# Optimization experiments

Measured on AMD Instinct MI355X. Metric: run time of the kernel, lower is better.

The kernel has to match this reference:

```python
import jax, jax.numpy as jnp
import numpy as np

B, S, H = 2, 2048, 2048
NH, NKV, HD = 16, 4, 128
EPS = 1e-6


def setup_inputs() -> dict:
    key = jax.random.key(0)
    ks = jax.random.split(key, 8)
    s = 0.02
    x = jax.random.normal(ks[0], (B, S, H), dtype=jnp.float32)
    # real rotary tables: cos/sin of shape [S, HD]
    inv_freq = 1.0 / (10000.0 ** (np.arange(0, HD, 2, dtype=np.float32) / HD))
    t = np.arange(S, dtype=np.float32)
    freqs = np.outer(t, inv_freq)              # [S, HD/2]
    emb = np.concatenate([freqs, freqs], axis=-1)  # [S, HD]
    rotary_cos = jnp.asarray(np.cos(emb))
    rotary_sin = jnp.asarray(np.sin(emb))
    Wq = jax.random.normal(ks[1], (H, NH * HD), dtype=jnp.float32) * s
    Wk = jax.random.normal(ks[2], (H, NKV * HD), dtype=jnp.float32) * s
    Wv = jax.random.normal(ks[3], (H, NKV * HD), dtype=jnp.float32) * s
    Wo = jax.random.normal(ks[4], (H, H), dtype=jnp.float32) * s
    q_norm_w = jnp.ones((HD,), dtype=jnp.float32)
    k_norm_w = jnp.ones((HD,), dtype=jnp.float32)
    return {"x": x, "rotary_cos": rotary_cos, "rotary_sin": rotary_sin,
            "Wq": Wq, "Wk": Wk, "Wv": Wv, "Wo": Wo,
            "q_norm_w": q_norm_w, "k_norm_w": k_norm_w}


def _rms_norm(x, w):
    return x * jax.lax.rsqrt(jnp.mean(x * x, axis=-1, keepdims=True) + EPS) * w


def _rotate_half(x):
    half = x.shape[-1] // 2
    return jnp.concatenate([-x[..., half:], x[..., :half]], axis=-1)


def reference(x, rotary_cos, rotary_sin, Wq, Wk, Wv, Wo, q_norm_w, k_norm_w):
    b, s, _ = x.shape
    q = (x @ Wq).reshape(b, s, NH, HD)
    k = (x @ Wk).reshape(b, s, NKV, HD)
    v = (x @ Wv).reshape(b, s, NKV, HD)
    q = _rms_norm(q, q_norm_w)
    k = _rms_norm(k, k_norm_w)
    cos = rotary_cos[None, :, None, :]  # [1,S,1,HD]
    sin = rotary_sin[None, :, None, :]
    q = q * cos + _rotate_half(q) * sin
    k = k * cos + _rotate_half(k) * sin
    # GQA: repeat kv heads
    rep = NH // NKV
    k = jnp.repeat(k, rep, axis=2)  # [b,s,NH,HD]
    v = jnp.repeat(v, rep, axis=2)
    scores = jnp.einsum('bqhd,bkhd->bhqk', q, k) / jnp.sqrt(jnp.float32(HD))
    causal = jnp.tril(jnp.ones((s, s), dtype=bool))
    scores = jnp.where(causal[None, None], scores, -jnp.inf)
    probs = jax.nn.softmax(scores.astype(jnp.float32), axis=-1).astype(q.dtype)
    y = jnp.einsum('bhqk,bkhd->bqhd', probs, v).reshape(b, s, NH * HD)
    return y @ Wo
```

## Files before the change

### kernel.cpp

```cpp
#include <hip/hip_runtime.h>


#define S_LEN 2048

typedef __bf16 bf16_t;
typedef bf16_t bf16x8 __attribute__((ext_vector_type(8)));
typedef float f32x4 __attribute__((ext_vector_type(4)));
typedef float f32x16 __attribute__((ext_vector_type(16)));
typedef unsigned int u32x4 __attribute__((ext_vector_type(4)));
typedef unsigned short u16x4 __attribute__((ext_vector_type(4)));

__device__ __forceinline__ unsigned short f2bf(float f) {
  unsigned int u = __builtin_bit_cast(unsigned int, f);
  u += 0x7fffu + ((u >> 16) & 1u);
  return (unsigned short)(u >> 16);
}
__device__ __forceinline__ float bf2f(unsigned short h) {
  return __builtin_bit_cast(float, (unsigned int)h << 16);
}
__device__ __forceinline__ unsigned pk2(float a, float b) {
  return (unsigned)f2bf(a) | ((unsigned)f2bf(b) << 16);
}
__device__ __forceinline__ unsigned cvtpk(float a, float b) {
  unsigned r;
  asm("v_cvt_pk_bf16_f32 %0, %1, %2" : "=v"(r) : "v"(a), "v"(b));
  return r;
}

typedef const __attribute__((address_space(1))) unsigned int* gas1_t;
typedef __attribute__((address_space(3))) unsigned int* las3_t;
__device__ __forceinline__ void async16(const void* g, void* l) {
  __builtin_amdgcn_global_load_lds((gas1_t)g, (las3_t)l, 16, 0, 0);
}

__device__ __forceinline__ bf16x8 ldfrag(const void* p) {
  return __builtin_bit_cast(bf16x8, *(const u32x4*)p);
}
__device__ __forceinline__ f32x16 mfma32(bf16x8 a, bf16x8 b, f32x16 c) {
  return __builtin_amdgcn_mfma_f32_32x32x16_bf16(a, b, c, 0, 0, 0);
}
__device__ __forceinline__ f32x16 zero16() {
  f32x16 v;
#pragma unroll
  for (int i = 0; i < 16; i++) v[i] = 0.f;
  return v;
}

__device__ __forceinline__ void transpose_body(
    const float* __restrict__ in, unsigned short* __restrict__ out,
    int C, int out_row_off, int out_ld, int bx, int by, int t,
    unsigned short (*L)[68]) {
  int r0 = by * 64, c0 = bx * 64;
#pragma unroll
  for (int i = 0; i < 4; i++) {
    int r = i * 16 + (t >> 4);
    int c = (t & 15) * 4;
    f32x4 v = *(const f32x4*)&in[(size_t)(r0 + r) * C + c0 + c];
    u16x4 u;
    u.x = f2bf(v.x); u.y = f2bf(v.y); u.z = f2bf(v.z); u.w = f2bf(v.w);
    *(u16x4*)&L[r][c] = u;
  }
  __syncthreads();
#pragma unroll
  for (int i = 0; i < 4; i++) {
    int oc = i * 16 + (t >> 4);
    int orr = (t & 15) * 4;
    u16x4 u;
    u.x = L[orr + 0][oc]; u.y = L[orr + 1][oc];
    u.z = L[orr + 2][oc]; u.w = L[orr + 3][oc];
    *(u16x4*)&out[(size_t)(c0 + oc + out_row_off) * out_ld + r0 + orr] = u;
  }
}

__global__ __launch_bounds__(256) void prep_kernel(
    const float* __restrict__ x, const float* __restrict__ Wq,
    const float* __restrict__ Wk, const float* __restrict__ Wv,
    const float* __restrict__ Wo, unsigned short* __restrict__ xb,
    unsigned short* __restrict__ WT, unsigned short* __restrict__ WoT) {
  __shared__ unsigned short L[64][68];
  const int bid = blockIdx.x, t = threadIdx.x;
  if (bid < 4096) {
    int i = bid * 256 + t;
    const f32x4* p = (const f32x4*)x + (size_t)i * 2;
    f32x4 a = p[0], b = p[1];
    u32x4 o;
    o.x = pk2(a.x, a.y);
    o.y = pk2(a.z, a.w);
    o.z = pk2(b.x, b.y);
    o.w = pk2(b.z, b.w);
    *(u32x4*)(xb + (size_t)i * 8) = o;
  } else if (bid < 5120) {
    int id = bid - 4096;
    transpose_body(Wq, WT, 2048, 0, 2048, id & 31, id >> 5, t, L);
  } else if (bid < 5376) {
    int id = bid - 5120;
    transpose_body(Wk, WT, 512, 2048, 2048, id & 7, id >> 3, t, L);
  } else if (bid < 5632) {
    int id = bid - 5376;
    transpose_body(Wv, WT, 512, 2560, 2048, id & 7, id >> 3, t, L);
  } else {
    int id = bid - 5632;
    transpose_body(Wo, WoT, 2048, 0, 2048, id & 31, id >> 5, t, L);
  }
}

__global__ __launch_bounds__(256) void gemm_bf16_kernel(
    const unsigned short* __restrict__ A, const unsigned short* __restrict__ Bt,
    void* __restrict__ Cout, int M, int N, int K, int NBX, int out_bf16,
    const float* __restrict__ cosT, const float* __restrict__ sinT,
    const float* __restrict__ qw, const float* __restrict__ kw,
    unsigned short* __restrict__ Qpk, unsigned short* __restrict__ Kpk,
    unsigned short* __restrict__ Vpk) {
  __shared__ __attribute__((aligned(16))) unsigned short shbuf[24576];
  unsigned short* As = shbuf;
  unsigned short* Bs = shbuf + 12288;
  const int t = threadIdx.x, w = t >> 6, l = t & 63;
  const int wr = w >> 1, wc = w & 1;
  const int lrow = l & 15, lhi = l >> 4;
  const int nb = gridDim.x;
  const int nsw = (blockIdx.x & 7) * (nb >> 3) + (blockIdx.x >> 3);
  const int bx = nsw % NBX, by = nsw / NBX;
  const int row0 = by * 128, col0 = bx * 128;
  const unsigned short* Ab = A + (size_t)row0 * K;
  const unsigned short* Bb = Bt + (size_t)col0 * K;
  const int srow = w * 32 + (l >> 2);
  const int scol = (l & 3) * 8;
  f32x4 z = {0.f, 0.f, 0.f, 0.f};
  f32x4 acc[4][4];
#pragma unroll
  for (int m = 0; m < 4; m++)
#pragma unroll
    for (int n = 0; n < 4; n++) acc[m][n] = z;

#define STAGE_G(tt, buf)                                                        \
  {                                                                             \
    const int k0_ = (tt) * 32;                                                  \
    async16(Ab + (size_t)srow * K + k0_ + scol,        &As[(buf) * 4096 + (w * 32) * 32]); \
    async16(Ab + (size_t)(srow + 16) * K + k0_ + scol, &As[(buf) * 4096 + (w * 32 + 16) * 32]); \
    async16(Bb + (size_t)srow * K + k0_ + scol,        &Bs[(buf) * 4096 + (w * 32) * 32]); \
    async16(Bb + (size_t)(srow + 16) * K + k0_ + scol, &Bs[(buf) * 4096 + (w * 32 + 16) * 32]); \
  }

  const int NT = K >> 5;
  STAGE_G(0, 0);
  for (int tt = 0; tt < NT; tt++) {
    const int cur = tt % 3;
    if (tt + 1 < NT) {
      STAGE_G(tt + 1, (tt + 1) % 3);
      asm volatile("s_waitcnt vmcnt(4)" ::: "memory");
    } else {
      asm volatile("s_waitcnt vmcnt(0)" ::: "memory");
    }
    __builtin_amdgcn_s_barrier();
    __builtin_amdgcn_sched_barrier(0);
    bf16x8 af[4], bfr[4];
#pragma unroll
    for (int m = 0; m < 4; m++)
      af[m] = ldfrag(&As[cur * 4096 + (wr * 64 + m * 16 + lrow) * 32 + lhi * 8]);
#pragma unroll
    for (int n = 0; n < 4; n++)
      bfr[n] = ldfrag(&Bs[cur * 4096 + (wc * 64 + n * 16 + lrow) * 32 + lhi * 8]);
    __builtin_amdgcn_s_setprio(1);
#pragma unroll
    for (int m = 0; m < 4; m++)
#pragma unroll
      for (int n = 0; n < 4; n++)
        acc[m][n] = __builtin_amdgcn_mfma_f32_16x16x32_bf16(af[m], bfr[n], acc[m][n], 0, 0, 0);
    __builtin_amdgcn_s_setprio(0);
  }
#undef STAGE_G

  if (Qpk) {
    __syncthreads();
#pragma unroll
    for (int m = 0; m < 4; m++)
#pragma unroll
      for (int n = 0; n < 4; n++)
#pragma unroll
        for (int r = 0; r < 4; r++)
          shbuf[(wr * 64 + m * 16 + lhi * 4 + r) * 132 + wc * 64 + n * 16 + lrow] =
              f2bf(acc[m][n][r]);
    __syncthreads();
    const int head = bx;
    const int d0 = 2 * l;
    for (int rr = 0; rr < 32; rr++) {
      const int row = w * 32 + rr;
      const int bs = row0 + row;
      const int b = bs >> 11, s = bs & 2047;
      unsigned int uu = *(const unsigned int*)&shbuf[row * 132 + d0];
      float x0 = bf2f((unsigned short)(uu & 0xffffu));
      float x1 = bf2f((unsigned short)(uu >> 16));
      if (head < 20) {
        const float* nw = (head < 16) ? qw : kw;
        float ss = x0 * x0 + x1 * x1;
#pragma unroll
        for (int mk = 1; mk < 64; mk <<= 1) ss += __shfl_xor(ss, mk);
        float inv = rsqrtf(ss * (1.0f / 128.0f) + 1e-6f);
        float n0 = x0 * inv * nw[d0], n1 = x1 * inv * nw[d0 + 1];
        float p0 = __shfl_xor(n0, 32), p1 = __shfl_xor(n1, 32);
        float sg = (l < 32) ? -1.0f : 1.0f;
        float c0 = cosT[s * 128 + d0], c1 = cosT[s * 128 + d0 + 1];
        float sn0 = sinT[s * 128 + d0], sn1 = sinT[s * 128 + d0 + 1];
        float o0 = n0 * c0 + sg * p0 * sn0;
        float o1 = n1 * c1 + sg * p1 * sn1;
        int mf = d0 >> 4, hi = (d0 >> 3) & 1, j = d0 & 7;
        int blk = s >> 5, r31 = s & 31;
        int foff = (mf * 2 + hi) * 256 + r31 * 8 + j;
        unsigned short* dst;
        if (head < 16) {
          const float qs = 0.08838834764831845f * 1.4426950408889634f;
          o0 *= qs; o1 *= qs;
          dst = Qpk + (((size_t)(b * 16 + head)) * 64 + blk) * 4096 + foff;
        } else {
          dst = Kpk + (((size_t)(b * 4 + (head - 16))) * 64 + blk) * 4096 + foff;
        }
        *(unsigned int*)dst = pk2(o0, o1);
      } else {
        int kvh = head - 20;
        int blk = s >> 5, ks = (s >> 4) & 1, his = (s >> 3) & 1, j = s & 7;
        int n = d0 >> 5, d31 = d0 & 31;
        size_t base = (((size_t)(b * 4 + kvh)) * 64 + blk) * 4096 +
                      (((n * 2 + ks) * 2 + his) * 256 + d31 * 8 + j);
        Vpk[base] = f2bf(x0);
        Vpk[base + 8] = f2bf(x1);
      }
    }
  } else if (out_bf16) {
    unsigned short* C = (unsigned short*)Cout;
#pragma unroll
    for (int m = 0; m < 4; m++)
#pragma unroll
      for (int n = 0; n < 4; n++)
#pragma unroll
        for (int r = 0; r < 4; r++) {
          size_t grow = row0 + wr * 64 + m * 16 + lhi * 4 + r;
          size_t gcol = col0 + wc * 64 + n * 16 + lrow;
          C[grow * N + gcol] = f2bf(acc[m][n][r]);
        }
  } else {
    float* C = (float*)Cout;
#pragma unroll
    for (int m = 0; m < 4; m++)
#pragma unroll
      for (int n = 0; n < 4; n++)
#pragma unroll
        for (int r = 0; r < 4; r++) {
          size_t grow = row0 + wr * 64 + m * 16 + lhi * 4 + r;
          size_t gcol = col0 + wc * 64 + n * 16 + lrow;
          C[grow * N + gcol] = acc[m][n][r];
        }
  }
}

__global__ __launch_bounds__(512) void attn_kernel(
    const unsigned short* __restrict__ Qpk, const unsigned short* __restrict__ Kpk,
    const unsigned short* __restrict__ Vpk, unsigned short* __restrict__ Y) {
  __shared__ __attribute__((aligned(16))) unsigned char lds_raw[100352];
  const int t = threadIdx.x, w = t >> 6, l = t & 63;
  const int q31 = l & 31, hi = l >> 5;
  const int grp = w >> 2, hw = w & 3;
  const int bid = blockIdx.x;
  const int xcd = bid & 7;
  const int b = xcd >> 2, kvh = xcd & 3;
  const int hd = kvh * 4 + hw;
  const int bh = b * 16 + hd;
  const int pj = bid >> 3;
  const unsigned short* Kg = Kpk + (size_t)(b * 4 + kvh) * 262144;
  const unsigned short* Vg = Vpk + (size_t)(b * 4 + kvh) * 262144;
  float* mlb = (float*)(lds_raw + 98304);

#define STAGE1(st, buf)                                                        \
  {                                                                            \
    unsigned char* base_ = lds_raw + ((buf) * 2 + grp) * 16384;                \
    const unsigned short* kg_ = Kg + (size_t)(st) * 4096;                      \
    const unsigned short* vg_ = Vg + (size_t)(st) * 4096;                      \
    _Pragma("unroll")                                                          \
    for (int i_ = 0; i_ < 4; i_++) {                                           \
      int c_ = hw * 4 + i_;                                                    \
      const unsigned short* src_ = (c_ < 8) ? (kg_ + c_ * 512 + l * 8)         \
                                            : (vg_ + (c_ - 8) * 512 + l * 8);  \
      async16(src_, base_ + c_ * 1024 + l * 16);                               \
    }                                                                          \
  }

  for (int phase = 0; phase < 2; phase++) {
    const int strip = phase ? pj : (63 - pj);
    const int q0w = strip * 32;
    const int qg = q0w + q31;
    const int nt = strip + 1;
    const int hcut = (nt + 1) >> 1;
    const int myFirst = grp ? hcut : 0;
    const int myCnt = grp ? (nt - hcut) : hcut;
    const int R = hcut;

    const unsigned short* Qs = Qpk + (((size_t)bh * 64 + strip) * 4096) + (size_t)l * 8;
    bf16x8 qf[8];
#pragma unroll
    for (int mf = 0; mf < 8; mf++) qf[mf] = ldfrag(Qs + mf * 512);
    asm volatile("s_waitcnt vmcnt(0)" ::: "memory");

    { int st0 = (myCnt > 0) ? myFirst : 0; STAGE1(st0, 0); }

    f32x16 o[4];
#pragma unroll
    for (int n = 0; n < 4; n++) o[n] = zero16();
    float m = -3.0e38f, lsum = 0.f;

    for (int r = 0; r < R; r++) {
      const int buf = r % 3;
      { int st = (r + 1 < myCnt) ? (myFirst + r + 1) : 0; STAGE1(st, (r + 1) % 3); }
      asm volatile("s_waitcnt vmcnt(4)" ::: "memory");
      __builtin_amdgcn_s_barrier();
      __builtin_amdgcn_sched_barrier(0);

      if (r < myCnt) {
        const int ti = myFirst + r;
        const int kv0 = ti << 5;
        const unsigned short* base =
            (const unsigned short*)(lds_raw + (buf * 2 + grp) * 16384);
        f32x16 sA = zero16(), sB = zero16();
        __builtin_amdgcn_s_setprio(1);
#pragma unroll
        for (int mf = 0; mf < 4; mf++) {
          sA = mfma32(ldfrag(base + mf * 512 + l * 8), qf[mf], sA);
          sB = mfma32(ldfrag(base + (mf + 4) * 512 + l * 8), qf[mf + 4], sB);
        }
        __builtin_amdgcn_s_setprio(0);
#pragma unroll
        for (int rr = 0; rr < 16; rr++) sA[rr] += sB[rr];
        if (ti == nt - 1) {
#pragma unroll
          for (int rr = 0; rr < 16; rr++) {
            int kv = kv0 + (rr & 3) + 8 * (rr >> 2) + 4 * hi;
            if (kv > qg) sA[rr] = -3.0e38f;
          }
        }
        float a0 = fmaxf(sA[0], sA[1]),   a1 = fmaxf(sA[2], sA[3]);
        float a2 = fmaxf(sA[4], sA[5]),   a3 = fmaxf(sA[6], sA[7]);
        float a4 = fmaxf(sA[8], sA[9]),   a5 = fmaxf(sA[10], sA[11]);
        float a6 = fmaxf(sA[12], sA[13]), a7 = fmaxf(sA[14], sA[15]);
        a0 = fmaxf(fmaxf(a0, a1), a2);
        a3 = fmaxf(fmaxf(a3, a4), a5);
        a6 = fmaxf(a6, a7);
        float pm = fmaxf(fmaxf(a0, a3), a6);
        pm = fmaxf(pm, __shfl_xor(pm, 32));
        if (__any(pm > m + 8.0f)) {
          float mn = fmaxf(m, pm);
          float scl = exp2f(m - mn);
          m = mn; lsum *= scl;
#pragma unroll
          for (int rr = 0; rr < 16; rr++) {
            float sr = __shfl(scl, (rr & 3) + 8 * (rr >> 2) + 4 * hi);
            o[0][rr] *= sr; o[1][rr] *= sr; o[2][rr] *= sr; o[3][rr] *= sr;
          }
        }
#pragma unroll
        for (int rr = 0; rr < 16; rr++) sA[rr] = exp2f(sA[rr] - m);
        float s0 = (sA[0] + sA[1]) + (sA[2] + sA[3]);
        float s1 = (sA[4] + sA[5]) + (sA[6] + sA[7]);
        float s2 = (sA[8] + sA[9]) + (sA[10] + sA[11]);
        float s3 = (sA[12] + sA[13]) + (sA[14] + sA[15]);
        float ts = (s0 + s1) + (s2 + s3);
        ts += __shfl_xor(ts, 32);
        lsum += ts;
        bf16x8 paf[2];
#pragma unroll
        for (int f = 0; f < 2; f++) {
          const int bs8 = 8 * f;
          unsigned g00 = cvtpk(sA[bs8 + 0], sA[bs8 + 1]);
          unsigned g01 = cvtpk(sA[bs8 + 2], sA[bs8 + 3]);
          unsigned g10 = cvtpk(sA[bs8 + 4], sA[bs8 + 5]);
          unsigned g11 = cvtpk(sA[bs8 + 6], sA[bs8 + 7]);
          unsigned snd0 = hi ? g00 : g10;
          unsigned snd1 = hi ? g01 : g11;
          unsigned r0 = (unsigned)__shfl_xor((int)snd0, 32);
          unsigned r1 = (unsigned)__shfl_xor((int)snd1, 32);
          unsigned own0 = hi ? g10 : g00;
          unsigned own1 = hi ? g11 : g01;
          u32x4 wv;
          wv.x = hi ? r0 : own0;
          wv.y = hi ? r1 : own1;
          wv.z = hi ? own0 : r0;
          wv.w = hi ? own1 : r1;
          paf[f] = __builtin_bit_cast(bf16x8, wv);
        }
        __builtin_amdgcn_s_setprio(1);
#pragma unroll
        for (int n = 0; n < 4; n++) {
          o[n] = mfma32(paf[0], ldfrag(base + 4096 + (n * 2 + 0) * 512 + l * 8), o[n]);
          o[n] = mfma32(paf[1], ldfrag(base + 4096 + (n * 2 + 1) * 512 + l * 8), o[n]);
        }
        __builtin_amdgcn_s_setprio(0);
      }
    }

    __syncthreads();
    if (l < 32) {
      mlb[hw * 128 + grp * 64 + q31] = m;
      mlb[hw * 128 + grp * 64 + 32 + q31] = lsum;
    }
    __syncthreads();
    float m_o = mlb[hw * 128 + (grp ^ 1) * 64 + q31];
    float l_o = mlb[hw * 128 + (grp ^ 1) * 64 + 32 + q31];
    float M = fmaxf(m, m_o);
    float sc = exp2f(m - M);
    float lF = lsum * sc + l_o * exp2f(m_o - M);
#pragma unroll
    for (int rr = 0; rr < 16; rr++) {
      float sr = __shfl(sc, (rr & 3) + 8 * (rr >> 2) + 4 * hi);
      o[0][rr] *= sr; o[1][rr] *= sr; o[2][rr] *= sr; o[3][rr] *= sr;
    }
    float* ob = (float*)lds_raw + hw * 4096;
    if (grp == 1) {
#pragma unroll
      for (int rr = 0; rr < 16; rr++) {
        int cr = (rr & 3) + 8 * (rr >> 2) + 4 * hi;
#pragma unroll
        for (int n = 0; n < 4; n++) ob[cr * 128 + n * 32 + q31] = o[n][rr];
      }
    }
    __syncthreads();
    if (grp == 0) {
      float linv = 1.0f / lF;
#pragma unroll
      for (int rr = 0; rr < 16; rr++) {
        int cr = (rr & 3) + 8 * (rr >> 2) + 4 * hi;
        float lr = __shfl(linv, cr);
        int qrow = q0w + cr;
        size_t rowoff = ((size_t)(b * S_LEN + qrow)) * 2048 + hd * 128 + q31;
        Y[rowoff]      = f2bf((o[0][rr] + ob[cr * 128 + q31]) * lr);
        Y[rowoff + 32] = f2bf((o[1][rr] + ob[cr * 128 + 32 + q31]) * lr);
        Y[rowoff + 64] = f2bf((o[2][rr] + ob[cr * 128 + 64 + q31]) * lr);
        Y[rowoff + 96] = f2bf((o[3][rr] + ob[cr * 128 + 96 + q31]) * lr);
      }
    }
    __syncthreads();
  }
#undef STAGE1
}

extern "C" void kernel_launch(void* const* d_in, const int* in_sizes, int n_in,
                              void* d_out, int out_size, void* d_ws, size_t ws_size,
                              hipStream_t stream) {
  const float* x  = (const float*)d_in[0];
  const float* rc = (const float*)d_in[1];
  const float* rs = (const float*)d_in[2];
  const float* Wq = (const float*)d_in[3];
  const float* Wk = (const float*)d_in[4];
  const float* Wv = (const float*)d_in[5];
  const float* Wo = (const float*)d_in[6];
  const float* qw = (const float*)d_in[7];
  const float* kw = (const float*)d_in[8];
  float* out = (float*)d_out;
  char* ws = (char*)d_ws;

  unsigned short* xb   = (unsigned short*)(ws + 0);
  unsigned short* WT   = (unsigned short*)(ws + 16777216);
  unsigned short* WoT  = (unsigned short*)(ws + 29360128);
  unsigned short* Qpk  = (unsigned short*)(ws + 37748736);
  unsigned short* Kpk  = (unsigned short*)(ws + 54525952);
  unsigned short* Vpk  = (unsigned short*)(ws + 58720256);
  unsigned short* Yb   = (unsigned short*)(ws + 0);

  prep_kernel<<<6656, 256, 0, stream>>>(x, Wq, Wk, Wv, Wo, xb, WT, WoT);
  gemm_bf16_kernel<<<768, 256, 0, stream>>>(
      xb, WT, nullptr, 4096, 3072, 2048, 24, 1, rc, rs, qw, kw, Qpk, Kpk, Vpk);
  attn_kernel<<<256, 512, 0, stream>>>(Qpk, Kpk, Vpk, Yb);
  gemm_bf16_kernel<<<512, 256, 0, stream>>>(
      Yb, WoT, out, 4096, 2048, 2048, 16, 0, nullptr, nullptr, nullptr, nullptr,
      nullptr, nullptr, nullptr);
}
```

Measured before the change: 208.5 us.

## Replace output projection GEMM with single-wave 64x64 tile kernel

Adds a new GEMM kernel in which each 64-thread block computes a 64x64 output tile, double-buffering K-slices of 32 in LDS with async loads and waiting on vmcnt instead of block barriers. The output projection launches 2048 of these small blocks instead of 512 larger 256-thread blocks. The aim is more blocks across the CUs and no workgroup synchronisation. The trade-off is less data reuse per tile, so more global and L2 traffic, and fewer waves per CU to hide latency.

New measurement: 223.2 us. 1.07x slower.

```diff
diff --git a/kernel.cpp b/kernel.cpp
--- a/kernel.cpp
+++ b/kernel.cpp
@@ -252,6 +252,76 @@
   }
 }
 
+__global__ __launch_bounds__(64) void gemm1w_kernel(
+    const unsigned short* __restrict__ A, const unsigned short* __restrict__ Bt,
+    float* __restrict__ C, int M, int N, int K, int NBX) {
+  __shared__ __attribute__((aligned(16))) unsigned short As[2][2048];
+  __shared__ __attribute__((aligned(16))) unsigned short Bs[2][2048];
+  const int l = threadIdx.x;
+  const int lrow = l & 15, lhi = l >> 4;
+  const int nb = gridDim.x;
+  const int nsw = (blockIdx.x & 7) * (nb >> 3) + (blockIdx.x >> 3);
+  const int bx = nsw % NBX, by = nsw / NBX;
+  const int row0 = by * 64, col0 = bx * 64;
+  const unsigned short* Ab = A + (size_t)row0 * K;
+  const unsigned short* Bb = Bt + (size_t)col0 * K;
+  const int srow = l >> 2;
+  const int scol = (l & 3) * 8;
+  f32x4 z = {0.f, 0.f, 0.f, 0.f};
+  f32x4 acc[4][4];
+#pragma unroll
+  for (int m = 0; m < 4; m++)
+#pragma unroll
+    for (int n = 0; n < 4; n++) acc[m][n] = z;
+
+#define STG1(tt, buf)                                                          \
+  {                                                                            \
+    const int k0_ = (tt) * 32;                                                 \
+    _Pragma("unroll")                                                          \
+    for (int i_ = 0; i_ < 4; i_++) {                                           \
+      async16(Ab + (size_t)(i_ * 16 + srow) * K + k0_ + scol, &As[buf][i_ * 512 + l * 8]); \
+      async16(Bb + (size_t)(i_ * 16 + srow) * K + k0_ + scol, &Bs[buf][i_ * 512 + l * 8]); \
+    }                                                                          \
+  }
+
+  const int NT = K >> 5;
+  STG1(0, 0);
+  for (int tt = 0; tt < NT; tt++) {
+    const int cur = tt & 1;
+    if (tt + 1 < NT) {
+      STG1(tt + 1, cur ^ 1);
+      asm volatile("s_waitcnt vmcnt(8)" ::: "memory");
+    } else {
+      asm volatile("s_waitcnt vmcnt(0)" ::: "memory");
+    }
+    bf16x8 af[4], bfr[4];
+#pragma unroll
+    for (int m = 0; m < 4; m++)
+      af[m] = ldfrag(&As[cur][(m * 16 + lrow) * 32 + lhi * 8]);
+#pragma unroll
+    for (int n = 0; n < 4; n++)
+      bfr[n] = ldfrag(&Bs[cur][(n * 16 + lrow) * 32 + lhi * 8]);
+#pragma unroll
+    for (int m = 0; m < 4; m++)
+#pragma unroll
+      for (int n = 0; n < 4; n++)
+        acc[m][n] = __builtin_amdgcn_mfma_f32_16x16x32_bf16(af[m], bfr[n], acc[m][n], 0, 0, 0);
+    __builtin_amdgcn_sched_barrier(0);
+  }
+#undef STG1
+
+#pragma unroll
+  for (int m = 0; m < 4; m++)
+#pragma unroll
+    for (int n = 0; n < 4; n++)
+#pragma unroll
+      for (int r = 0; r < 4; r++) {
+        size_t grow = row0 + m * 16 + lhi * 4 + r;
+        size_t gcol = col0 + n * 16 + lrow;
+        C[grow * N + gcol] = acc[m][n][r];
+      }
+}
+
 __global__ __launch_bounds__(512) void attn_kernel(
     const unsigned short* __restrict__ Qpk, const unsigned short* __restrict__ Kpk,
     const unsigned short* __restrict__ Vpk, unsigned short* __restrict__ Y) {
@@ -466,7 +536,5 @@
   gemm_bf16_kernel<<<768, 256, 0, stream>>>(
       xb, WT, nullptr, 4096, 3072, 2048, 24, 1, rc, rs, qw, kw, Qpk, Kpk, Vpk);
   attn_kernel<<<256, 512, 0, stream>>>(Qpk, Kpk, Vpk, Yb);
-  gemm_bf16_kernel<<<512, 256, 0, stream>>>(
-      Yb, WoT, out, 4096, 2048, 2048, 16, 0, nullptr, nullptr, nullptr, nullptr,
-      nullptr, nullptr, nullptr);
-}
+  gemm1w_kernel<<<2048, 64, 0, stream>>>(Yb, WoT, out, 4096, 2048, 2048, 32);
+}
```
